# Optimization experiments

Measured on AMD Instinct MI355X. Metric: run time of the kernel, lower is better.

Reference implementation:

```python
import jax, jax.numpy as jnp
import numpy as np
from jax import lax

B, CIN, COUT, CS, K, KSZ, L = 64, 256, 256, 256, 4, 3, 1024
HIDDEN = CS // 4          # ratio = 4
TEMPERATURE = 30.0


def setup_inputs() -> dict:
    key = jax.random.key(0)
    k0, k1, k2, k3, k4, k5 = jax.random.split(key, 6)
    x = jax.random.normal(k0, (B, CIN, L, 1), dtype=jnp.float32)
    cond = jax.random.normal(k1, (B, CS), dtype=jnp.float32)
    # attention MLP (1x1 convs == dense layers on (B, C))
    w1 = jax.random.normal(k2, (HIDDEN, CS), dtype=jnp.float32) * (2.0 / CS) ** 0.5
    w2 = jax.random.normal(k3, (K, HIDDEN), dtype=jnp.float32) * (2.0 / HIDDEN) ** 0.5
    # K expert kernels and biases
    weight = jax.random.normal(k4, (K, COUT, CIN, KSZ, KSZ), dtype=jnp.float32) * 0.05
    bias = jax.random.normal(k5, (K, COUT), dtype=jnp.float32) * 0.05
    return {"x": x, "cond": cond, "w1": w1, "w2": w2, "weight": weight, "bias": bias}


def reference(x, cond, w1, w2, weight, bias):
    # Attention routing: softmax over K mixture logits (temperature-scaled)
    logits = jax.nn.relu(cond @ w1.T) @ w2.T          # (B, K)
    att = jax.nn.softmax(logits / TEMPERATURE, axis=-1)
    # Per-sample aggregated kernel / bias (mixture of K experts)
    agg_w = jnp.einsum('bk,koihw->boihw', att, weight)  # (B, COUT, CIN, 3, 3)
    agg_b = att @ bias                                  # (B, COUT)
    # Per-sample conv2d (stride 1, padding 1) — vmap replaces the groups=B trick
    def conv_one(xi, wi):
        y = lax.conv_general_dilated(
            xi[None], wi, window_strides=(1, 1), padding=[(1, 1), (1, 1)],
            dimension_numbers=('NCHW', 'OIHW', 'NCHW'))
        return y[0]
    out = jax.vmap(conv_one)(x, agg_w)                  # (B, COUT, L, 1)
    return out + agg_b[:, :, None, None]
```

## Files before the change

kernel.cpp:

```cpp
#include <hip/hip_runtime.h>

typedef __attribute__((ext_vector_type(8))) short bf16x8;
typedef __attribute__((ext_vector_type(4))) short s16x4;
typedef __attribute__((ext_vector_type(4))) float f32x4;

#define B_SZ   64
#define CIN    256
#define COUT   256
#define CS     256
#define HIDDEN 64
#define L_SZ   1024
#define LPAD   1026
#define TEMP   30.0f

#define OFF_ATT   0u
#define OFF_AGGB  1024u
#define OFF_WAGG  66560u
#define OFF_XBF   25232384u

__device__ __forceinline__ unsigned short f2bf(float f) {
    union { float f; unsigned int u; } v; v.f = f;
    unsigned int u = v.u;
    return (unsigned short)((u + 0x7fffu + ((u >> 16) & 1u)) >> 16);
}

__device__ __forceinline__ void load_lds16(const unsigned short* g, unsigned short* l) {
    __builtin_amdgcn_global_load_lds(
        (const __attribute__((address_space(1))) unsigned int*)g,
        (__attribute__((address_space(3))) unsigned int*)l, 16, 0, 0);
}

__global__ void routing_kernel(const float* __restrict__ cond,
                               const float* __restrict__ w1,
                               const float* __restrict__ w2,
                               const float* __restrict__ bias,
                               float* __restrict__ att_g,
                               float* __restrict__ aggb_g,
                               unsigned short* __restrict__ xbf) {
    __shared__ float cond_s[CS];
    __shared__ float h_s[HIDDEN];
    __shared__ float lg_s[4];
    int t = threadIdx.x;
    int b = blockIdx.x;
    cond_s[t] = cond[b * CS + t];
    xbf[(size_t)b * LPAD * CIN + t] = 0;
    xbf[((size_t)b * LPAD + (LPAD - 1)) * CIN + t] = 0;
    __syncthreads();
    int jj = t >> 2, s = t & 3;
    float p = 0.f;
    const float* w1r = w1 + jj * CS + s * 64;
    const float* cs  = cond_s + s * 64;
    #pragma unroll 16
    for (int c = 0; c < 64; ++c) p += cs[c] * w1r[c];
    p += __shfl_down(p, 2, 4);
    p += __shfl_down(p, 1, 4);
    if (s == 0) h_s[jj] = fmaxf(p, 0.f);
    __syncthreads();
    if (t < 4) {
        float z = 0.f;
        #pragma unroll 16
        for (int h = 0; h < HIDDEN; ++h) z += h_s[h] * w2[t * HIDDEN + h];
        lg_s[t] = z * (1.0f / TEMP);
    }
    __syncthreads();
    float l0 = lg_s[0], l1 = lg_s[1], l2 = lg_s[2], l3 = lg_s[3];
    float mx = fmaxf(fmaxf(l0, l1), fmaxf(l2, l3));
    float e0 = __expf(l0 - mx), e1 = __expf(l1 - mx);
    float e2 = __expf(l2 - mx), e3 = __expf(l3 - mx);
    float inv = 1.0f / (e0 + e1 + e2 + e3);
    float a0 = e0 * inv, a1 = e1 * inv, a2 = e2 * inv, a3 = e3 * inv;
    if (t == 0) {
        att_g[b * 4 + 0] = a0; att_g[b * 4 + 1] = a1;
        att_g[b * 4 + 2] = a2; att_g[b * 4 + 3] = a3;
    }
    aggb_g[b * COUT + t] = a0 * bias[0 * COUT + t] + a1 * bias[1 * COUT + t]
                         + a2 * bias[2 * COUT + t] + a3 * bias[3 * COUT + t];
}

__global__ __launch_bounds__(256)
void xpose_kernel(const float* __restrict__ x,
                  unsigned short* __restrict__ xbf) {
    __shared__ __align__(16) unsigned short tile[64 * 264];
    int lt = blockIdx.x, b = blockIdx.y;
    int t = threadIdx.x;
    int w = t >> 6, lane = t & 63;
    int sub = lane & 15, grp = lane >> 4;
    const float4* xp4 = (const float4*)x;
    #pragma unroll
    for (int it = 0; it < 4; ++it) {
        #pragma unroll
        for (int j = 0; j < 4; ++j) {
            int i_loc = it * 64 + w * 16 + j * 4 + grp;
            float4 v = xp4[((size_t)(b * CIN + i_loc)) * (L_SZ / 4) + lt * 16 + sub];
            { float a = (grp & 1) ? v.x : v.y;
              float c = (grp & 1) ? v.z : v.w;
              float ra = __shfl_xor(a, 16);
              float rc = __shfl_xor(c, 16);
              if (grp & 1) { v.x = ra; v.z = rc; } else { v.y = ra; v.w = rc; } }
            { float a  = (grp & 2) ? v.x : v.z;
              float b2 = (grp & 2) ? v.y : v.w;
              float ra = __shfl_xor(a, 32);
              float rb = __shfl_xor(b2, 32);
              if (grp & 2) { v.x = ra; v.y = rb; } else { v.z = ra; v.w = rb; } }
            int l_loc = sub * 4 + grp;
            s16x4 pk;
            pk.x = (short)f2bf(v.x); pk.y = (short)f2bf(v.y);
            pk.z = (short)f2bf(v.z); pk.w = (short)f2bf(v.w);
            *(s16x4*)&tile[l_loc * 264 + it * 64 + w * 16 + j * 4] = pk;
        }
    }
    __syncthreads();
    int half = lane >> 5, c16 = lane & 31;
    unsigned short* dstb = xbf + ((size_t)b * LPAD + lt * 64 + 1) * CIN;
    #pragma unroll
    for (int rr = 0; rr < 16; rr += 2) {
        int row = w * 16 + rr + half;
        bf16x8 vv = *(const bf16x8*)&tile[row * 264 + c16 * 8];
        *(bf16x8*)&dstb[(size_t)row * CIN + c16 * 8] = vv;
    }
}

__global__ void wagg_kernel(const float* __restrict__ weight,
                            const float* __restrict__ att_g,
                            unsigned short* __restrict__ wagg) {
    __shared__ float w_s[4][2304];
    __shared__ float att_s[256];
    int o = blockIdx.x;
    int t = threadIdx.x;
    att_s[t] = att_g[t];
    #pragma unroll
    for (int k = 0; k < 4; ++k) {
        const float4* src = (const float4*)(weight + ((size_t)k * COUT + o) * 2304);
        for (int idx = t; idx < 576; idx += 256)
            *(float4*)&w_s[k][idx * 4] = src[idx];
    }
    __syncthreads();
    int i2 = (t & 127) * 2, half = t >> 7;
    float wv[3][2][4];
    #pragma unroll
    for (int kh = 0; kh < 3; ++kh)
        #pragma unroll
        for (int d = 0; d < 2; ++d)
            #pragma unroll
            for (int k = 0; k < 4; ++k)
                wv[kh][d][k] = w_s[k][(i2 + d) * 9 + kh * 3 + 1];
    for (int bb = half * 32; bb < half * 32 + 32; ++bb) {
        float a0 = att_s[bb * 4 + 0], a1 = att_s[bb * 4 + 1];
        float a2 = att_s[bb * 4 + 2], a3 = att_s[bb * 4 + 3];
        #pragma unroll
        for (int kh = 0; kh < 3; ++kh) {
            float v0 = wv[kh][0][0] * a0 + wv[kh][0][1] * a1
                     + wv[kh][0][2] * a2 + wv[kh][0][3] * a3;
            float v1 = wv[kh][1][0] * a0 + wv[kh][1][1] * a1
                     + wv[kh][1][2] * a2 + wv[kh][1][3] * a3;
            ushort2 pk; pk.x = f2bf(v0); pk.y = f2bf(v1);
            *(ushort2*)&wagg[(((size_t)bb * 3 + kh) * COUT + o) * CIN + i2] = pk;
        }
    }
}

__global__ __launch_bounds__(256, 4)
void dynconv_gemm(const unsigned short* __restrict__ wagg,
                  const unsigned short* __restrict__ xbf,
                  const float* __restrict__ aggb,
                  float* __restrict__ out) {
    __shared__ __align__(16) unsigned char smem[33792];
    unsigned short* As = (unsigned short*)smem;
    unsigned short* Bs = (unsigned short*)(smem + 24576);
    float* Cs = (float*)smem;
    int bx = blockIdx.x;
    int r8 = bx & 7, s = bx >> 3;
    int tile = s & 15, q = s >> 4;
    int b = r8 + 8 * q;
    int mt = tile & 1, nt = tile >> 1;
    int l0 = nt * 128, m0 = mt * 128;
    int t = threadIdx.x;
    int w = t >> 6, lane = t & 63;
    int ln = lane & 15, hi = lane >> 4;
    int wm = w & 1, wn = w >> 1;
    int jq = lane >> 2, jc = lane & 3;
    int gc = jc ^ ((jq >> 1) & 3);

    f32x4 acc[4][4];
    #pragma unroll
    for (int a = 0; a < 4; ++a)
        #pragma unroll
        for (int c = 0; c < 4; ++c) acc[a][c] = (f32x4){0.f, 0.f, 0.f, 0.f};

    const unsigned short* wb = wagg + (size_t)b * 3 * COUT * CIN;
    const unsigned short* xb = xbf + (size_t)b * LPAD * CIN;

    for (int it = 0; it < 8; ++it) {
        int i0 = it * 32;
        #pragma unroll
        for (int si = 0; si < 6; ++si) {
            int inst = w * 6 + si;
            int R = inst * 16 + jq;
            int kh = R >> 7, m = R & 127;
            const unsigned short* g =
                wb + ((size_t)(kh * COUT + m0 + m)) * CIN + i0 + gc * 8;
            load_lds16(g, &As[inst * 512]);
        }
        for (int bi = w; bi < 9; bi += 4) {
            int r = bi * 16 + jq;
            if (r < 130) {
                const unsigned short* g = xb + (size_t)(l0 + r) * CIN + i0 + gc * 8;
                load_lds16(g, &Bs[bi * 512]);
            }
        }
        __syncthreads();
        #pragma unroll
        for (int kh = 0; kh < 3; ++kh) {
            bf16x8 af[4], bfr[4];
            #pragma unroll
            for (int mi = 0; mi < 4; ++mi) {
                int m = wm * 64 + mi * 16 + ln;
                af[mi] = *(const bf16x8*)&As[kh * 4096 + m * 32 + (hi ^ ((m >> 1) & 3)) * 8];
            }
            #pragma unroll
            for (int ni = 0; ni < 4; ++ni) {
                int r = wn * 64 + ni * 16 + ln + kh;
                bfr[ni] = *(const bf16x8*)&Bs[r * 32 + (hi ^ ((r >> 1) & 3)) * 8];
            }
            #pragma unroll
            for (int mi = 0; mi < 4; ++mi)
                #pragma unroll
                for (int ni = 0; ni < 4; ++ni)
                    acc[mi][ni] = __builtin_amdgcn_mfma_f32_16x16x32_bf16(
                        af[mi], bfr[ni], acc[mi][ni], 0, 0, 0);
        }
        __syncthreads();
    }

    const float* abb = aggb + b * COUT;
    float* ob = out + (size_t)b * COUT * L_SZ;
    #pragma unroll
    for (int p = 0; p < 2; ++p) {
        __syncthreads();
        if (wm == p) {
            #pragma unroll
            for (int mi = 0; mi < 4; ++mi)
                #pragma unroll
                for (int reg = 0; reg < 4; ++reg) {
                    int r = mi * 16 + hi * 4 + reg;
                    float bv = abb[m0 + p * 64 + r];
                    #pragma unroll
                    for (int ni = 0; ni < 4; ++ni)
                        Cs[r * 132 + wn * 64 + ni * 16 + ln] = acc[mi][ni][reg] + bv;
                }
        }
        __syncthreads();
        #pragma unroll
        for (int v = 0; v < 8; ++v) {
            int idx4 = v * 256 + t;
            int row = idx4 >> 5;
            int c4 = idx4 & 31;
            f32x4 val = *(const f32x4*)&Cs[row * 132 + c4 * 4];
            *(f32x4*)&ob[(size_t)(m0 + p * 64 + row) * L_SZ + l0 + c4 * 4] = val;
        }
    }
}

extern "C" void kernel_launch(void* const* d_in, const int* in_sizes, int n_in,
                              void* d_out, int out_size, void* d_ws, size_t ws_size,
                              hipStream_t stream) {
    const float* x      = (const float*)d_in[0];
    const float* cond   = (const float*)d_in[1];
    const float* w1     = (const float*)d_in[2];
    const float* w2     = (const float*)d_in[3];
    const float* weight = (const float*)d_in[4];
    const float* bias   = (const float*)d_in[5];
    float* out = (float*)d_out;
    char* ws = (char*)d_ws;
    float* att_g  = (float*)(ws + OFF_ATT);
    float* aggb_g = (float*)(ws + OFF_AGGB);
    unsigned short* wagg = (unsigned short*)(ws + OFF_WAGG);
    unsigned short* xbf  = (unsigned short*)(ws + OFF_XBF);

    routing_kernel<<<64, 256, 0, stream>>>(cond, w1, w2, bias, att_g, aggb_g, xbf);
    xpose_kernel<<<dim3(16, 64), 256, 0, stream>>>(x, xbf);
    wagg_kernel<<<256, 256, 0, stream>>>(weight, att_g, wagg);
    dynconv_gemm<<<1024, 256, 0, stream>>>(wagg, xbf, aggb_g, out);
}
```

Baseline: 179.8 us.

## Double-buffer GEMM LDS loads and merge transpose and weight-aggregation kernels

```diff
diff --git a/kernel.cpp b/kernel.cpp
--- a/kernel.cpp
+++ b/kernel.cpp
@@ -78,96 +78,95 @@
 }
 
 __global__ __launch_bounds__(256)
-void xpose_kernel(const float* __restrict__ x,
-                  unsigned short* __restrict__ xbf) {
-    __shared__ __align__(16) unsigned short tile[64 * 264];
-    int lt = blockIdx.x, b = blockIdx.y;
+void prep_kernel(const float* __restrict__ x,
+                 const float* __restrict__ weight,
+                 const float* __restrict__ att_g,
+                 unsigned short* __restrict__ xbf,
+                 unsigned short* __restrict__ wagg) {
+    __shared__ __align__(16) unsigned char sm[37888];
+    int bx = blockIdx.x;
     int t = threadIdx.x;
-    int w = t >> 6, lane = t & 63;
-    int sub = lane & 15, grp = lane >> 4;
-    const float4* xp4 = (const float4*)x;
-    #pragma unroll
-    for (int it = 0; it < 4; ++it) {
-        #pragma unroll
-        for (int j = 0; j < 4; ++j) {
-            int i_loc = it * 64 + w * 16 + j * 4 + grp;
-            float4 v = xp4[((size_t)(b * CIN + i_loc)) * (L_SZ / 4) + lt * 16 + sub];
-            { float a = (grp & 1) ? v.x : v.y;
-              float c = (grp & 1) ? v.z : v.w;
-              float ra = __shfl_xor(a, 16);
-              float rc = __shfl_xor(c, 16);
-              if (grp & 1) { v.x = ra; v.z = rc; } else { v.y = ra; v.w = rc; } }
-            { float a  = (grp & 2) ? v.x : v.z;
-              float b2 = (grp & 2) ? v.y : v.w;
-              float ra = __shfl_xor(a, 32);
-              float rb = __shfl_xor(b2, 32);
-              if (grp & 2) { v.x = ra; v.y = rb; } else { v.z = ra; v.w = rb; } }
-            int l_loc = sub * 4 + grp;
-            s16x4 pk;
-            pk.x = (short)f2bf(v.x); pk.y = (short)f2bf(v.y);
-            pk.z = (short)f2bf(v.z); pk.w = (short)f2bf(v.w);
-            *(s16x4*)&tile[l_loc * 264 + it * 64 + w * 16 + j * 4] = pk;
-        }
-    }
-    __syncthreads();
-    int half = lane >> 5, c16 = lane & 31;
-    unsigned short* dstb = xbf + ((size_t)b * LPAD + lt * 64 + 1) * CIN;
-    #pragma unroll
-    for (int rr = 0; rr < 16; rr += 2) {
-        int row = w * 16 + rr + half;
-        bf16x8 vv = *(const bf16x8*)&tile[row * 264 + c16 * 8];
-        *(bf16x8*)&dstb[(size_t)row * CIN + c16 * 8] = vv;
-    }
-}
-
-__global__ void wagg_kernel(const float* __restrict__ weight,
-                            const float* __restrict__ att_g,
-                            unsigned short* __restrict__ wagg) {
-    __shared__ float w_s[4][2304];
-    __shared__ float att_s[256];
-    int o = blockIdx.x;
-    int t = threadIdx.x;
-    att_s[t] = att_g[t];
-    #pragma unroll
-    for (int k = 0; k < 4; ++k) {
-        const float4* src = (const float4*)(weight + ((size_t)k * COUT + o) * 2304);
-        for (int idx = t; idx < 576; idx += 256)
-            *(float4*)&w_s[k][idx * 4] = src[idx];
-    }
-    __syncthreads();
-    int i2 = (t & 127) * 2, half = t >> 7;
-    float wv[3][2][4];
-    #pragma unroll
-    for (int kh = 0; kh < 3; ++kh)
-        #pragma unroll
-        for (int d = 0; d < 2; ++d)
-            #pragma unroll
-            for (int k = 0; k < 4; ++k)
-                wv[kh][d][k] = w_s[k][(i2 + d) * 9 + kh * 3 + 1];
-    for (int bb = half * 32; bb < half * 32 + 32; ++bb) {
-        float a0 = att_s[bb * 4 + 0], a1 = att_s[bb * 4 + 1];
-        float a2 = att_s[bb * 4 + 2], a3 = att_s[bb * 4 + 3];
-        #pragma unroll
-        for (int kh = 0; kh < 3; ++kh) {
-            float v0 = wv[kh][0][0] * a0 + wv[kh][0][1] * a1
-                     + wv[kh][0][2] * a2 + wv[kh][0][3] * a3;
-            float v1 = wv[kh][1][0] * a0 + wv[kh][1][1] * a1
-                     + wv[kh][1][2] * a2 + wv[kh][1][3] * a3;
-            ushort2 pk; pk.x = f2bf(v0); pk.y = f2bf(v1);
-            *(ushort2*)&wagg[(((size_t)bb * 3 + kh) * COUT + o) * CIN + i2] = pk;
-        }
-    }
-}
-
-__global__ __launch_bounds__(256, 4)
+    if (bx < 1024) {
+        unsigned short* tile = (unsigned short*)sm;
+        int lt = bx & 15, b = bx >> 4;
+        int w = t >> 6, lane = t & 63;
+        int sub = lane & 15, grp = lane >> 4;
+        const float4* xp4 = (const float4*)x;
+        #pragma unroll
+        for (int it = 0; it < 4; ++it) {
+            #pragma unroll
+            for (int j = 0; j < 4; ++j) {
+                int i_loc = it * 64 + w * 16 + j * 4 + grp;
+                float4 v = xp4[((size_t)(b * CIN + i_loc)) * (L_SZ / 4) + lt * 16 + sub];
+                { float a = (grp & 1) ? v.x : v.y;
+                  float c = (grp & 1) ? v.z : v.w;
+                  float ra = __shfl_xor(a, 16);
+                  float rc = __shfl_xor(c, 16);
+                  if (grp & 1) { v.x = ra; v.z = rc; } else { v.y = ra; v.w = rc; } }
+                { float a  = (grp & 2) ? v.x : v.z;
+                  float b2 = (grp & 2) ? v.y : v.w;
+                  float ra = __shfl_xor(a, 32);
+                  float rb = __shfl_xor(b2, 32);
+                  if (grp & 2) { v.x = ra; v.y = rb; } else { v.z = ra; v.w = rb; } }
+                int l_loc = sub * 4 + grp;
+                s16x4 pk;
+                pk.x = (short)f2bf(v.x); pk.y = (short)f2bf(v.y);
+                pk.z = (short)f2bf(v.z); pk.w = (short)f2bf(v.w);
+                *(s16x4*)&tile[l_loc * 264 + it * 64 + w * 16 + j * 4] = pk;
+            }
+        }
+        __syncthreads();
+        int half = lane >> 5, c16 = lane & 31;
+        unsigned short* dstb = xbf + ((size_t)b * LPAD + lt * 64 + 1) * CIN;
+        #pragma unroll
+        for (int rr = 0; rr < 16; rr += 2) {
+            int row = w * 16 + rr + half;
+            bf16x8 vv = *(const bf16x8*)&tile[row * 264 + c16 * 8];
+            *(bf16x8*)&dstb[(size_t)row * CIN + c16 * 8] = vv;
+        }
+    } else {
+        float* w_s   = (float*)sm;
+        float* att_s = (float*)(sm + 36864);
+        int o = bx - 1024;
+        att_s[t] = att_g[t];
+        #pragma unroll
+        for (int k = 0; k < 4; ++k) {
+            const float4* src = (const float4*)(weight + ((size_t)k * COUT + o) * 2304);
+            for (int idx = t; idx < 576; idx += 256)
+                *(float4*)&w_s[k * 2304 + idx * 4] = src[idx];
+        }
+        __syncthreads();
+        int i2 = (t & 127) * 2, half = t >> 7;
+        float wv[3][2][4];
+        #pragma unroll
+        for (int kh = 0; kh < 3; ++kh)
+            #pragma unroll
+            for (int d = 0; d < 2; ++d)
+                #pragma unroll
+                for (int k = 0; k < 4; ++k)
+                    wv[kh][d][k] = w_s[k * 2304 + (i2 + d) * 9 + kh * 3 + 1];
+        for (int bb = half * 32; bb < half * 32 + 32; ++bb) {
+            float a0 = att_s[bb * 4 + 0], a1 = att_s[bb * 4 + 1];
+            float a2 = att_s[bb * 4 + 2], a3 = att_s[bb * 4 + 3];
+            #pragma unroll
+            for (int kh = 0; kh < 3; ++kh) {
+                float v0 = wv[kh][0][0] * a0 + wv[kh][0][1] * a1
+                         + wv[kh][0][2] * a2 + wv[kh][0][3] * a3;
+                float v1 = wv[kh][1][0] * a0 + wv[kh][1][1] * a1
+                         + wv[kh][1][2] * a2 + wv[kh][1][3] * a3;
+                ushort2 pk; pk.x = f2bf(v0); pk.y = f2bf(v1);
+                *(ushort2*)&wagg[(((size_t)bb * 3 + kh) * COUT + o) * CIN + i2] = pk;
+            }
+        }
+    }
+}
+
+__global__ __launch_bounds__(256, 2)
 void dynconv_gemm(const unsigned short* __restrict__ wagg,
                   const unsigned short* __restrict__ xbf,
                   const float* __restrict__ aggb,
                   float* __restrict__ out) {
-    __shared__ __align__(16) unsigned char smem[33792];
-    unsigned short* As = (unsigned short*)smem;
-    unsigned short* Bs = (unsigned short*)(smem + 24576);
-    float* Cs = (float*)smem;
+    __shared__ __align__(16) unsigned char smem[67584];
     int bx = blockIdx.x;
     int r8 = bx & 7, s = bx >> 3;
     int tile = s & 15, q = s >> 4;
@@ -190,25 +189,31 @@
     const unsigned short* wb = wagg + (size_t)b * 3 * COUT * CIN;
     const unsigned short* xb = xbf + (size_t)b * LPAD * CIN;
 
-    for (int it = 0; it < 8; ++it) {
+    auto issue = [&](int it, int buf) {
         int i0 = it * 32;
+        unsigned short* As_ = (unsigned short*)(smem + buf * 33792);
+        unsigned short* Bs_ = (unsigned short*)(smem + buf * 33792 + 24576);
         #pragma unroll
         for (int si = 0; si < 6; ++si) {
             int inst = w * 6 + si;
             int R = inst * 16 + jq;
             int kh = R >> 7, m = R & 127;
-            const unsigned short* g =
-                wb + ((size_t)(kh * COUT + m0 + m)) * CIN + i0 + gc * 8;
-            load_lds16(g, &As[inst * 512]);
+            load_lds16(wb + ((size_t)(kh * COUT + m0 + m)) * CIN + i0 + gc * 8,
+                       &As_[inst * 512]);
         }
         for (int bi = w; bi < 9; bi += 4) {
             int r = bi * 16 + jq;
-            if (r < 130) {
-                const unsigned short* g = xb + (size_t)(l0 + r) * CIN + i0 + gc * 8;
-                load_lds16(g, &Bs[bi * 512]);
-            }
-        }
+            if (r < 130)
+                load_lds16(xb + (size_t)(l0 + r) * CIN + i0 + gc * 8, &Bs_[bi * 512]);
+        }
+    };
+
+    issue(0, 0);
+    for (int it = 0; it < 8; ++it) {
         __syncthreads();
+        if (it < 7) issue(it + 1, (it + 1) & 1);
+        const unsigned short* As = (const unsigned short*)(smem + (it & 1) * 33792);
+        const unsigned short* Bs = (const unsigned short*)(smem + (it & 1) * 33792 + 24576);
         #pragma unroll
         for (int kh = 0; kh < 3; ++kh) {
             bf16x8 af[4], bfr[4];
@@ -229,35 +234,30 @@
                     acc[mi][ni] = __builtin_amdgcn_mfma_f32_16x16x32_bf16(
                         af[mi], bfr[ni], acc[mi][ni], 0, 0, 0);
         }
-        __syncthreads();
-    }
-
+    }
+    __syncthreads();
+
+    float* Cs = (float*)smem;
     const float* abb = aggb + b * COUT;
+    #pragma unroll
+    for (int mi = 0; mi < 4; ++mi)
+        #pragma unroll
+        for (int reg = 0; reg < 4; ++reg) {
+            int r = wm * 64 + mi * 16 + hi * 4 + reg;
+            float bv = abb[m0 + r];
+            #pragma unroll
+            for (int ni = 0; ni < 4; ++ni)
+                Cs[r * 132 + wn * 64 + ni * 16 + ln] = acc[mi][ni][reg] + bv;
+        }
+    __syncthreads();
     float* ob = out + (size_t)b * COUT * L_SZ;
     #pragma unroll
-    for (int p = 0; p < 2; ++p) {
-        __syncthreads();
-        if (wm == p) {
-            #pragma unroll
-            for (int mi = 0; mi < 4; ++mi)
-                #pragma unroll
-                for (int reg = 0; reg < 4; ++reg) {
-                    int r = mi * 16 + hi * 4 + reg;
-                    float bv = abb[m0 + p * 64 + r];
-                    #pragma unroll
-                    for (int ni = 0; ni < 4; ++ni)
-                        Cs[r * 132 + wn * 64 + ni * 16 + ln] = acc[mi][ni][reg] + bv;
-                }
-        }
-        __syncthreads();
-        #pragma unroll
-        for (int v = 0; v < 8; ++v) {
-            int idx4 = v * 256 + t;
-            int row = idx4 >> 5;
-            int c4 = idx4 & 31;
-            f32x4 val = *(const f32x4*)&Cs[row * 132 + c4 * 4];
-            *(f32x4*)&ob[(size_t)(m0 + p * 64 + row) * L_SZ + l0 + c4 * 4] = val;
-        }
+    for (int v = 0; v < 16; ++v) {
+        int idx4 = v * 256 + t;
+        int row = idx4 >> 5;
+        int c4 = idx4 & 31;
+        f32x4 val = *(const f32x4*)&Cs[row * 132 + c4 * 4];
+        *(f32x4*)&ob[(size_t)(m0 + row) * L_SZ + l0 + c4 * 4] = val;
     }
 }
 
@@ -278,7 +278,6 @@
     unsigned short* xbf  = (unsigned short*)(ws + OFF_XBF);
 
     routing_kernel<<<64, 256, 0, stream>>>(cond, w1, w2, bias, att_g, aggb_g, xbf);
-    xpose_kernel<<<dim3(16, 64), 256, 0, stream>>>(x, xbf);
-    wagg_kernel<<<256, 256, 0, stream>>>(weight, att_g, wagg);
+    prep_kernel<<<1280, 256, 0, stream>>>(x, weight, att_g, xbf, wagg);
     dynconv_gemm<<<1024, 256, 0, stream>>>(wagg, xbf, aggb_g, out);
 }
```

Measured after the change: 181.8 us. About the same (+1.1%).
